# Kernel optimization log

Measured on AMD Instinct MI355X. Metric: run time of the kernel, lower is better.

Reference implementation:

```python
import jax, jax.numpy as jnp
import numpy as np

B, S, HID, NH, INTER = 1, 2048, 1024, 16, 4096
D = INTER // NH  # per-head intermediate dim = 256


def setup_inputs() -> dict:
    key = jax.random.key(0)
    ks = jax.random.split(key, 10)
    w = lambda k, shp: jax.random.normal(k, shp, jnp.float32) * 0.02
    return {
        "x": jax.random.normal(ks[0], (B, S, HID), jnp.float32),
        "adjacency": jax.random.uniform(ks[1], (B, NH, S, S), jnp.float32),
        "Wg": w(ks[2], (INTER, HID)),   # gate_proj.weight (out,in)
        "Wu": w(ks[3], (INTER, HID)),   # up_proj.weight
        "Wd": w(ks[4], (HID, INTER)),   # down_proj.weight
        "eps": jnp.zeros((NH,), jnp.float32),   # GIN epsilons (init 0)
        "alpha": jnp.ones((NH,), jnp.float32),  # sum-agg scales (init 1)
        "Wq": w(ks[5], (NH, D, D)),     # per-head attn_query_projs weights (out,in)
        "Wk": w(ks[6], (NH, D, D)),     # per-head attn_key_projs weights
        "W1": w(ks[7], (D, 4 * D)),     # aggregator_mlp[0].weight
        "W2": w(ks[8], (D, D)),         # aggregator_mlp[2].weight
    }


def reference(x, adjacency, Wg, Wu, Wd, eps, alpha, Wq, Wk, W1, W2):
    b, s, _ = x.shape
    nh, d, _ = Wq.shape
    # first half of SwiGLU MLP
    h = jax.nn.silu(x @ Wg.T) * (x @ Wu.T)            # (b, s, inter)
    h = h.reshape(b, s, nh, d).transpose(0, 2, 1, 3)  # (b, h, s, d)
    # GIN original term
    orig = (1.0 + eps)[None, :, None, None] * h
    # sum aggregation over adjacency
    sum_agg = alpha[None, :, None, None] * jnp.einsum('bhij,bhjd->bhid', adjacency, h)
    # max over identical expanded copies of h along the neighbor axis == h itself
    max_agg = h
    # adjacency-log-masked attention aggregation
    Q = jnp.einsum('bhsd,hed->bhse', h, Wq)
    K = jnp.einsum('bhsd,hed->bhse', h, Wk)
    scores = jnp.einsum('bhse,bhte->bhst', Q, K) / jnp.sqrt(jnp.float32(d))
    scores = scores + jnp.log(adjacency + 1e-9)
    attn = jax.nn.softmax(scores, axis=-1)
    attn_agg = jnp.einsum('bhst,bhtd->bhsd', attn, h)
    # 4-way concat + aggregator MLP (per head, shared weights)
    comb = jnp.concatenate([orig, sum_agg, max_agg, attn_agg], axis=-1)  # (b,h,s,4d)
    gin = jnp.einsum('bhsd,od->bhso', jax.nn.silu(jnp.einsum('bhsi,oi->bhso', comb, W1)), W2)
    # recombine heads and finish MLP
    gin = gin.transpose(0, 2, 1, 3).reshape(b, s, nh * d)
    return gin @ Wd.T
```

## Files before the change

kernel.cpp:

```cpp
#include <hip/hip_runtime.h>

typedef unsigned short u16;
typedef __attribute__((ext_vector_type(4))) float f32x4;
typedef __attribute__((ext_vector_type(8))) short s16x8;
typedef __attribute__((ext_vector_type(4))) short s16x4;

#define DEVI static __device__ __forceinline__

constexpr int S = 2048, HID = 1024, NH = 16, D = 256, INTER = 4096;

constexpr size_t N_XB   = (size_t)S*HID;
constexpr size_t N_W    = (size_t)INTER*HID;
constexpr size_t N_WQK  = (size_t)NH*D*D;
constexpr size_t N_W1C  = (size_t)NH*D*768;
constexpr size_t N_W2   = (size_t)D*D;
constexpr size_t N_COMB = (size_t)NH*S*768;
constexpr size_t N_HB   = (size_t)NH*S*D;

constexpr size_t O_XB   = 0;
constexpr size_t O_WG   = O_XB + N_XB;
constexpr size_t O_WU   = O_WG + N_W;
constexpr size_t O_WD   = O_WU + N_W;
constexpr size_t O_WQ   = O_WD + N_W;
constexpr size_t O_WK   = O_WQ + N_WQK;
constexpr size_t O_W1C  = O_WK + N_WQK;
constexpr size_t O_W2   = O_W1C + N_W1C;
constexpr size_t O_COMB = O_W2 + N_W2;
constexpr size_t O_HB   = O_COMB + N_COMB;
constexpr size_t O_QB   = O_HB + N_HB;
constexpr size_t O_KC   = O_QB + N_HB;

DEVI u16 f2bf(float f) {
  union { float f; unsigned u; } v; v.f = f;
  unsigned r = v.u + 0x7FFFu + ((v.u >> 16) & 1u);
  return (u16)(r >> 16);
}

DEVI float bf2f(u16 b) {
  union { unsigned u; float f; } v; v.u = ((unsigned)b) << 16;
  return v.f;
}

DEVI void gload16(const void* g, const void* l) {
  __builtin_amdgcn_global_load_lds(
      (const __attribute__((address_space(1))) unsigned int*)g,
      (__attribute__((address_space(3))) unsigned int*)l, 16, 0, 0);
}

DEVI void stage_rm(const u16* src, int stride, u16* lds, int tid) {
  const int wid = tid >> 6;
#pragma unroll
  for (int i = 0; i < 2; ++i) {
    int c = i * 256 + tid;
    gload16(src + (size_t)(c & 127) * stride + (c >> 7) * 8,
            lds + (size_t)(i * 256 + wid * 64) * 8);
  }
}

DEVI s16x8 ldfrag(const u16* lds, int kp, int row) {
  return *(const s16x8*)(lds + ((size_t)kp * 128 + row) * 8);
}

__global__ void k_convert(const float* __restrict__ x,  const float* __restrict__ Wg,
                          const float* __restrict__ Wu, const float* __restrict__ Wd,
                          const float* __restrict__ Wq, const float* __restrict__ Wk,
                          const float* __restrict__ W1, const float* __restrict__ W2,
                          const float* __restrict__ eps, const float* __restrict__ alpha,
                          u16* __restrict__ ws) {
  const size_t total = N_XB + N_W + N_W + N_W + N_WQK + N_WQK + N_W2 + N_W1C;
  for (size_t i = (size_t)blockIdx.x * blockDim.x + threadIdx.x; i < total;
       i += (size_t)gridDim.x * blockDim.x) {
    size_t j = i;
    if (j < N_XB)  { ws[O_XB + j] = f2bf(x[j]);  continue; } j -= N_XB;
    if (j < N_W)   { ws[O_WG + j] = f2bf(Wg[j]); continue; } j -= N_W;
    if (j < N_W)   { ws[O_WU + j] = f2bf(Wu[j]); continue; } j -= N_W;
    if (j < N_W)   { ws[O_WD + j] = f2bf(Wd[j]); continue; } j -= N_W;
    if (j < N_WQK) { ws[O_WQ + j] = f2bf(Wq[j]); continue; } j -= N_WQK;
    if (j < N_WQK) { ws[O_WK + j] = f2bf(Wk[j]); continue; } j -= N_WQK;
    if (j < N_W2)  { ws[O_W2 + j] = f2bf(W2[(j % D) * D + (j / D)]); continue; } j -= N_W2;
    size_t h = j / ((size_t)D * 768);
    size_t r = j % ((size_t)D * 768);
    size_t o = r / 768, c = r % 768;
    float v;
    if (c < 256)      v = (1.f + eps[h]) * W1[o * 1024 + c] + W1[o * 1024 + 512 + c];
    else if (c < 512) v = alpha[h] * W1[o * 1024 + c];
    else              v = W1[o * 1024 + 256 + c];
    ws[O_W1C + j] = f2bf(v);
  }
}

template <int MODE>
__global__ __launch_bounds__(256, 2) void k_dual(const u16* __restrict__ Ab,
                                                 const u16* __restrict__ B0b,
                                                 const u16* __restrict__ B1b,
                                                 u16* __restrict__ o0, u16* __restrict__ o1) {
  __shared__ u16 lA[4096], lB0[4096], lB1[4096];
  const int tid = threadIdx.x, lane = tid & 63, wid = tid >> 6;
  const int wm = wid >> 1, wn = wid & 1;
  const int m0 = blockIdx.x * 128, nt = blockIdx.y, head = blockIdx.z;

  const int K  = (MODE == 0) ? HID : D;
  const int sA = (MODE == 0) ? HID : 768;
  const int sB = (MODE == 0) ? HID : D;
  const u16* A  = (MODE == 0) ? (Ab + (size_t)m0 * HID)
                              : (Ab + ((size_t)head * S + m0) * 768);
  const u16* B0 = (MODE == 0) ? (B0b + (size_t)nt * 128 * HID)
                              : (B0b + (size_t)head * D * D + (size_t)nt * 128 * D);
  const u16* B1 = (MODE == 0) ? (B1b + (size_t)nt * 128 * HID)
                              : (B1b + (size_t)head * D * D + (size_t)nt * 128 * D);

  f32x4 a0[4][4], a1[4][4];
#pragma unroll
  for (int i = 0; i < 4; ++i)
#pragma unroll
    for (int j = 0; j < 4; ++j) { a0[i][j] = f32x4{0.f,0.f,0.f,0.f}; a1[i][j] = f32x4{0.f,0.f,0.f,0.f}; }

  for (int k0 = 0; k0 < K; k0 += 32) {
    __syncthreads();
    stage_rm(A  + k0, sA, lA,  tid);
    stage_rm(B0 + k0, sB, lB0, tid);
    stage_rm(B1 + k0, sB, lB1, tid);
    __syncthreads();
    const int kp = lane >> 4, r = lane & 15;
    s16x8 af[4], b0f[4], b1f[4];
#pragma unroll
    for (int f = 0; f < 4; ++f) {
      af[f]  = ldfrag(lA,  kp, wm * 64 + f * 16 + r);
      b0f[f] = ldfrag(lB0, kp, wn * 64 + f * 16 + r);
      b1f[f] = ldfrag(lB1, kp, wn * 64 + f * 16 + r);
    }
#pragma unroll
    for (int fi = 0; fi < 4; ++fi)
#pragma unroll
      for (int fj = 0; fj < 4; ++fj) {
        a0[fi][fj] = __builtin_amdgcn_mfma_f32_16x16x32_bf16(af[fi], b0f[fj], a0[fi][fj], 0, 0, 0);
        a1[fi][fj] = __builtin_amdgcn_mfma_f32_16x16x32_bf16(af[fi], b1f[fj], a1[fi][fj], 0, 0, 0);
      }
  }

#pragma unroll
  for (int fi = 0; fi < 4; ++fi)
#pragma unroll
    for (int fj = 0; fj < 4; ++fj)
#pragma unroll
      for (int reg = 0; reg < 4; ++reg) {
        int row = m0 + wm * 64 + fi * 16 + ((lane >> 4) * 4 + reg);
        int cl  = wn * 64 + fj * 16 + (lane & 15);
        if (MODE == 0) {
          int col = nt * 128 + cl;
          float g = a0[fi][fj][reg], uu = a1[fi][fj][reg];
          float h = g / (1.f + __expf(-g)) * uu;
          u16 hb = f2bf(h);
          int hh = col >> 8, d = col & 255;
          o0[((size_t)hh * S + row) * 768 + d] = hb;
          o1[(((size_t)hh * (S / 8) + (row >> 3)) * 256 + d) * 8 + (row & 7)] = hb;
        } else {
          int e = nt * 128 + cl;
          o0[((size_t)head * S + row) * D + e] = f2bf(a0[fi][fj][reg]);
          o1[(((size_t)head * 32 + (e >> 3)) * S + row) * 8 + (e & 7)] = f2bf(a1[fi][fj][reg]);
        }
      }
}

__global__ __launch_bounds__(256, 2) void k_attn(const float* __restrict__ adj,
                                                 const u16* __restrict__ Qb,
                                                 const u16* __restrict__ Kc,
                                                 const u16* __restrict__ hB,
                                                 u16* __restrict__ comb) {
  __shared__ u16 lK[2][1024 * 8];
  __shared__ u16 lH[2][1024 * 8];
  __shared__ u16 lAdj[2][64 * 36];
  __shared__ u16 lP[4][16 * 36];
  const int tid = threadIdx.x, lane = tid & 63, wid = tid >> 6;
  const int head = blockIdx.y;
  const int q0 = blockIdx.x * 64 + wid * 16;
  const int l15 = lane & 15, l4 = lane >> 4;

  s16x8 q[8];
  {
    const u16* qr = Qb + ((size_t)head * S + q0 + l15) * D + l4 * 8;
#pragma unroll
    for (int ks = 0; ks < 8; ++ks) q[ks] = *(const s16x8*)(qr + ks * 32);
  }
  f32x4 accO[16], accS[16];
#pragma unroll
  for (int i = 0; i < 16; ++i) { accO[i] = f32x4{0.f,0.f,0.f,0.f}; accS[i] = f32x4{0.f,0.f,0.f,0.f}; }
  float m_r[4] = {-1e30f, -1e30f, -1e30f, -1e30f};
  float l_r[4] = {0.f, 0.f, 0.f, 0.f};

  const float* adjB = adj + ((size_t)head * S + blockIdx.x * 64) * S;
  const int arow = tid >> 3;
  const int acol = (tid & 7) * 4;

#pragma unroll
  for (int i = 0; i < 4; ++i) {
    int c = i * 256 + tid;
    gload16(Kc + ((size_t)(head * 32 + (c >> 5)) * S + (c & 31)) * 8,
            &lK[0][(size_t)(i * 256 + wid * 64) * 8]);
  }
#pragma unroll
  for (int i = 0; i < 4; ++i) {
    int c = i * 256 + tid;
    gload16(hB + ((size_t)(head * (S / 8) + (c >> 8)) * 256 + (c & 255)) * 8,
            &lH[0][(size_t)(i * 256 + wid * 64) * 8]);
  }
  f32x4 av0 = *(const f32x4*)(adjB + (size_t)arow * S + acol);
  f32x4 av1 = *(const f32x4*)(adjB + (size_t)(arow + 32) * S + acol);

  int cur = 0;
  for (int t0 = 0; t0 < S; t0 += 32, cur ^= 1) {
    const int t1 = (t0 + 32 < S) ? t0 + 32 : t0;
#pragma unroll
    for (int i = 0; i < 4; ++i) {
      int c = i * 256 + tid;
      gload16(Kc + ((size_t)(head * 32 + (c >> 5)) * S + t1 + (c & 31)) * 8,
              &lK[cur ^ 1][(size_t)(i * 256 + wid * 64) * 8]);
    }
#pragma unroll
    for (int i = 0; i < 4; ++i) {
      int c = i * 256 + tid;
      gload16(hB + ((size_t)(head * (S / 8) + (t1 >> 3) + (c >> 8)) * 256 + (c & 255)) * 8,
              &lH[cur ^ 1][(size_t)(i * 256 + wid * 64) * 8]);
    }
    f32x4 nv0 = *(const f32x4*)(adjB + (size_t)arow * S + t1 + acol);
    f32x4 nv1 = *(const f32x4*)(adjB + (size_t)(arow + 32) * S + t1 + acol);
    {
      s16x4 w;
      w[0] = (short)f2bf(av0[0]); w[1] = (short)f2bf(av0[1]);
      w[2] = (short)f2bf(av0[2]); w[3] = (short)f2bf(av0[3]);
      *(s16x4*)(&lAdj[cur][(size_t)arow * 36 + acol]) = w;
      w[0] = (short)f2bf(av1[0]); w[1] = (short)f2bf(av1[1]);
      w[2] = (short)f2bf(av1[2]); w[3] = (short)f2bf(av1[3]);
      *(s16x4*)(&lAdj[cur][(size_t)(arow + 32) * 36 + acol]) = w;
    }
    __builtin_amdgcn_sched_barrier(0);
    asm volatile("s_waitcnt vmcnt(10) lgkmcnt(0)" ::: "memory");
    __builtin_amdgcn_sched_barrier(0);
    __builtin_amdgcn_s_barrier();
    __builtin_amdgcn_sched_barrier(0);

    const u16* lKc = &lK[cur][0];
    const u16* lHc = &lH[cur][0];
    const u16* lAc = &lAdj[cur][0];

    f32x4 scA[2], scB[2];
    scA[0] = f32x4{0.f,0.f,0.f,0.f}; scA[1] = f32x4{0.f,0.f,0.f,0.f};
    scB[0] = f32x4{0.f,0.f,0.f,0.f}; scB[1] = f32x4{0.f,0.f,0.f,0.f};
    __builtin_amdgcn_s_setprio(1);
#pragma unroll
    for (int ks = 0; ks < 4; ++ks)
#pragma unroll
      for (int fj = 0; fj < 2; ++fj) {
        s16x8 b0 = *(const s16x8*)(lKc + ((size_t)(ks * 4 + l4) * 32 + fj * 16 + l15) * 8);
        s16x8 b1 = *(const s16x8*)(lKc + ((size_t)((ks + 4) * 4 + l4) * 32 + fj * 16 + l15) * 8);
        scA[fj] = __builtin_amdgcn_mfma_f32_16x16x32_bf16(q[ks], b0, scA[fj], 0, 0, 0);
        scB[fj] = __builtin_amdgcn_mfma_f32_16x16x32_bf16(q[ks + 4], b1, scB[fj], 0, 0, 0);
      }
    __builtin_amdgcn_s_setprio(0);

    float av[2][4];
#pragma unroll
    for (int fj = 0; fj < 2; ++fj)
#pragma unroll
      for (int reg = 0; reg < 4; ++reg)
        av[fj][reg] = bf2f(lAc[(size_t)(wid * 16 + l4 * 4 + reg) * 36 + fj * 16 + l15]);

    float sf[2][4];
#pragma unroll
    for (int fj = 0; fj < 2; ++fj)
#pragma unroll
      for (int reg = 0; reg < 4; ++reg)
        sf[fj][reg] = (scA[fj][reg] + scB[fj][reg]) * 0.0625f;

    bool chg = false;
    float lmax[4];
#pragma unroll
    for (int reg = 0; reg < 4; ++reg) {
      lmax[reg] = fmaxf(sf[0][reg], sf[1][reg]);
      chg |= (lmax[reg] > m_r[reg] + 8.f);
    }
    if (__any((int)chg)) {
      float scl[4];
#pragma unroll
      for (int reg = 0; reg < 4; ++reg) {
        float m = lmax[reg];
#pragma unroll
        for (int off = 1; off < 16; off <<= 1) m = fmaxf(m, __shfl_xor(m, off));
        float mn = fmaxf(m_r[reg], m);
        scl[reg] = __expf(m_r[reg] - mn);
        m_r[reg] = mn;
        l_r[reg] *= scl[reg];
      }
#pragma unroll
      for (int nf = 0; nf < 16; ++nf) {
        f32x4 t = accO[nf];
        t[0] *= scl[0]; t[1] *= scl[1]; t[2] *= scl[2]; t[3] *= scl[3];
        accO[nf] = t;
      }
    }
    u16 pb[2][4];
#pragma unroll
    for (int fj = 0; fj < 2; ++fj)
#pragma unroll
      for (int reg = 0; reg < 4; ++reg) {
        float p = (av[fj][reg] + 1e-9f) * exp2f((sf[fj][reg] - m_r[reg]) * 1.44269504f);
        l_r[reg] += p;
        pb[fj][reg] = f2bf(p);
      }

    u16* pl = &lP[wid][0];
#pragma unroll
    for (int fj = 0; fj < 2; ++fj)
#pragma unroll
      for (int reg = 0; reg < 4; ++reg)
        pl[(size_t)(l4 * 4 + reg) * 36 + fj * 16 + l15] = pb[fj][reg];
    asm volatile("s_waitcnt lgkmcnt(0)" ::: "memory");
    __builtin_amdgcn_sched_barrier(0);

    s16x8 pa, aa;
    {
      s16x4 plo = *(const s16x4*)(pl + (size_t)l15 * 36 + l4 * 8);
      s16x4 phi = *(const s16x4*)(pl + (size_t)l15 * 36 + l4 * 8 + 4);
      pa[0] = plo[0]; pa[1] = plo[1]; pa[2] = plo[2]; pa[3] = plo[3];
      pa[4] = phi[0]; pa[5] = phi[1]; pa[6] = phi[2]; pa[7] = phi[3];
      s16x4 alo = *(const s16x4*)(lAc + (size_t)(wid * 16 + l15) * 36 + l4 * 8);
      s16x4 ahi = *(const s16x4*)(lAc + (size_t)(wid * 16 + l15) * 36 + l4 * 8 + 4);
      aa[0] = alo[0]; aa[1] = alo[1]; aa[2] = alo[2]; aa[3] = alo[3];
      aa[4] = ahi[0]; aa[5] = ahi[1]; aa[6] = ahi[2]; aa[7] = ahi[3];
    }
    __builtin_amdgcn_s_setprio(1);
#pragma unroll
    for (int nf = 0; nf < 16; ++nf) {
      s16x8 hb = *(const s16x8*)(lHc + ((size_t)l4 * 256 + nf * 16 + l15) * 8);
      accO[nf] = __builtin_amdgcn_mfma_f32_16x16x32_bf16(pa, hb, accO[nf], 0, 0, 0);
      accS[nf] = __builtin_amdgcn_mfma_f32_16x16x32_bf16(aa, hb, accS[nf], 0, 0, 0);
    }
    __builtin_amdgcn_s_setprio(0);

    av0 = nv0; av1 = nv1;

    __builtin_amdgcn_sched_barrier(0);
    __builtin_amdgcn_s_barrier();
  }

  asm volatile("s_waitcnt vmcnt(0)" ::: "memory");

#pragma unroll
  for (int reg = 0; reg < 4; ++reg) {
#pragma unroll
    for (int off = 1; off < 16; off <<= 1) l_r[reg] += __shfl_xor(l_r[reg], off);
  }
  float inv[4];
#pragma unroll
  for (int reg = 0; reg < 4; ++reg) inv[reg] = 1.f / l_r[reg];
#pragma unroll
  for (int nf = 0; nf < 16; ++nf)
#pragma unroll
    for (int reg = 0; reg < 4; ++reg) {
      size_t rb = ((size_t)head * S + q0 + l4 * 4 + reg) * 768;
      comb[rb + 512 + nf * 16 + l15] = f2bf(accO[nf][reg] * inv[reg]);
      comb[rb + 256 + nf * 16 + l15] = f2bf(accS[nf][reg]);
    }
}

template <int MODE>
__global__ __launch_bounds__(256, 2) void k_gemm(const u16* __restrict__ Ab,
                                                 const u16* __restrict__ Bb,
                                                 u16* __restrict__ oU, float* __restrict__ oF) {
  __shared__ u16 lA[4096], lB[4096];
  const int tid = threadIdx.x, lane = tid & 63, wid = tid >> 6;
  const int wm = wid >> 1, wn = wid & 1;
  const int m0 = blockIdx.x * 128, nt = blockIdx.y, head = blockIdx.z;

  constexpr int K  = (MODE == 0) ? 768 : (MODE == 2) ? INTER : D;
  constexpr int sA = (MODE == 3) ? INTER : K;
  constexpr int sB = K;
  const u16* A = (MODE == 0) ? Ab + ((size_t)head * S + m0) * 768
               : (MODE == 2) ? Ab + (size_t)m0 * INTER
                             : Ab + (size_t)m0 * INTER + head * D;
  const u16* B = (MODE == 0) ? Bb + ((size_t)head * D + nt * 128) * 768
                             : Bb + (size_t)nt * 128 * sB;

  f32x4 acc[4][4];
#pragma unroll
  for (int i = 0; i < 4; ++i)
#pragma unroll
    for (int j = 0; j < 4; ++j) acc[i][j] = f32x4{0.f,0.f,0.f,0.f};

  for (int k0 = 0; k0 < K; k0 += 32) {
    __syncthreads();
    stage_rm(A + k0, sA, lA, tid);
    stage_rm(B + k0, sB, lB, tid);
    __syncthreads();
    const int kp = lane >> 4, r = lane & 15;
    s16x8 af[4], bf[4];
#pragma unroll
    for (int f = 0; f < 4; ++f) {
      af[f] = ldfrag(lA, kp, wm * 64 + f * 16 + r);
      bf[f] = ldfrag(lB, kp, wn * 64 + f * 16 + r);
    }
#pragma unroll
    for (int fi = 0; fi < 4; ++fi)
#pragma unroll
      for (int fj = 0; fj < 4; ++fj)
        acc[fi][fj] = __builtin_amdgcn_mfma_f32_16x16x32_bf16(af[fi], bf[fj], acc[fi][fj], 0, 0, 0);
  }

#pragma unroll
  for (int fi = 0; fi < 4; ++fi)
#pragma unroll
    for (int fj = 0; fj < 4; ++fj)
#pragma unroll
      for (int reg = 0; reg < 4; ++reg) {
        int row = m0 + wm * 64 + fi * 16 + ((lane >> 4) * 4 + reg);
        int cn = nt * 128 + wn * 64 + fj * 16 + (lane & 15);
        float v = acc[fi][fj][reg];
        if (MODE == 0) {
          v = v / (1.f + __expf(-v));
          oU[(size_t)row * INTER + head * D + cn] = f2bf(v);
        } else if (MODE == 3) {
          oU[(size_t)row * INTER + head * D + cn] = f2bf(v);
        } else {
          oF[(size_t)row * HID + cn] = v;
        }
      }
}

extern "C" void kernel_launch(void* const* d_in, const int* in_sizes, int n_in,
                              void* d_out, int out_size, void* d_ws, size_t ws_size,
                              hipStream_t stream) {
  const float* x     = (const float*)d_in[0];
  const float* adj   = (const float*)d_in[1];
  const float* Wg    = (const float*)d_in[2];
  const float* Wu    = (const float*)d_in[3];
  const float* Wd    = (const float*)d_in[4];
  const float* eps   = (const float*)d_in[5];
  const float* alpha = (const float*)d_in[6];
  const float* Wq    = (const float*)d_in[7];
  const float* Wk    = (const float*)d_in[8];
  const float* W1    = (const float*)d_in[9];
  const float* W2    = (const float*)d_in[10];
  u16* ws = (u16*)d_ws;

  k_convert<<<dim3(4096), dim3(256), 0, stream>>>(x, Wg, Wu, Wd, Wq, Wk, W1, W2, eps, alpha, ws);
  k_dual<0><<<dim3(16, 32, 1), dim3(256), 0, stream>>>(ws + O_XB, ws + O_WG, ws + O_WU,
                                                       ws + O_COMB, ws + O_HB);
  k_dual<1><<<dim3(16, 2, 16), dim3(256), 0, stream>>>(ws + O_COMB, ws + O_WQ, ws + O_WK,
                                                       ws + O_QB, ws + O_KC);
  k_attn<<<dim3(32, 16), dim3(256), 0, stream>>>(adj, ws + O_QB, ws + O_KC, ws + O_HB, ws + O_COMB);
  k_gemm<3><<<dim3(8, 2, 16), dim3(256), 0, stream>>>(ws + O_WD, ws + O_W2, ws + O_KC, nullptr);
  k_gemm<0><<<dim3(16, 2, 16), dim3(256), 0, stream>>>(ws + O_COMB, ws + O_W1C, ws + O_QB, nullptr);
  k_gemm<2><<<dim3(16, 8, 1), dim3(256), 0, stream>>>(ws + O_QB, ws + O_KC, nullptr, (float*)d_out);
}
```

Measured before the change: 449.4 us.

## Compute transposed scores to skip P LDS round-trip and drop online max

The attention kernel now computes S^T by swapping the MFMA operands, so each lane holds the scores in the layout needed for the P operand of the PV matmul. The probabilities are packed straight into registers with 16x16x16 MFMAs, which removes the per-wave LDS staging buffer and its wait. The running-max rescaling is also dropped and the exponentials are taken unshifted, on the assumption that scores stay small. This cuts ALU, shuffle and LDS work, but it doubles the MFMA instruction count and risks overflow if scores grow.

```diff
diff --git a/kernel.cpp b/kernel.cpp
--- a/kernel.cpp
+++ b/kernel.cpp
@@ -45,6 +45,19 @@
   __builtin_amdgcn_global_load_lds(
       (const __attribute__((address_space(1))) unsigned int*)g,
       (__attribute__((address_space(3))) unsigned int*)l, 16, 0, 0);
+}
+
+DEVI f32x4 mfma16(s16x4 a, s16x4 b, f32x4 c) {
+#if __has_builtin(__builtin_amdgcn_mfma_f32_16x16x16_bf16)
+  return __builtin_amdgcn_mfma_f32_16x16x16_bf16(a, b, c, 0, 0, 0);
+#elif __has_builtin(__builtin_amdgcn_mfma_f32_16x16x16bf16_1k)
+  return __builtin_amdgcn_mfma_f32_16x16x16bf16_1k(a, b, c, 0, 0, 0);
+#else
+  f32x4 d;
+  asm volatile("v_mfma_f32_16x16x16_bf16 %0, %1, %2, %3"
+               : "=v"(d) : "v"(a), "v"(b), "v"(c));
+  return d;
+#endif
 }
 
 DEVI void stage_rm(const u16* src, int stride, u16* lds, int tid) {
@@ -170,7 +183,6 @@
   __shared__ u16 lK[2][1024 * 8];
   __shared__ u16 lH[2][1024 * 8];
   __shared__ u16 lAdj[2][64 * 36];
-  __shared__ u16 lP[4][16 * 36];
   const int tid = threadIdx.x, lane = tid & 63, wid = tid >> 6;
   const int head = blockIdx.y;
   const int q0 = blockIdx.x * 64 + wid * 16;
@@ -185,8 +197,7 @@
   f32x4 accO[16], accS[16];
 #pragma unroll
   for (int i = 0; i < 16; ++i) { accO[i] = f32x4{0.f,0.f,0.f,0.f}; accS[i] = f32x4{0.f,0.f,0.f,0.f}; }
-  float m_r[4] = {-1e30f, -1e30f, -1e30f, -1e30f};
-  float l_r[4] = {0.f, 0.f, 0.f, 0.f};
+  float l_r = 0.f;
 
   const float* adjB = adj + ((size_t)head * S + blockIdx.x * 64) * S;
   const int arow = tid >> 3;
@@ -251,89 +262,36 @@
     for (int ks = 0; ks < 4; ++ks)
 #pragma unroll
       for (int fj = 0; fj < 2; ++fj) {
-        s16x8 b0 = *(const s16x8*)(lKc + ((size_t)(ks * 4 + l4) * 32 + fj * 16 + l15) * 8);
-        s16x8 b1 = *(const s16x8*)(lKc + ((size_t)((ks + 4) * 4 + l4) * 32 + fj * 16 + l15) * 8);
-        scA[fj] = __builtin_amdgcn_mfma_f32_16x16x32_bf16(q[ks], b0, scA[fj], 0, 0, 0);
-        scB[fj] = __builtin_amdgcn_mfma_f32_16x16x32_bf16(q[ks + 4], b1, scB[fj], 0, 0, 0);
+        s16x8 k0f = *(const s16x8*)(lKc + ((size_t)(ks * 4 + l4) * 32 + fj * 16 + l15) * 8);
+        s16x8 k1f = *(const s16x8*)(lKc + ((size_t)((ks + 4) * 4 + l4) * 32 + fj * 16 + l15) * 8);
+        scA[fj] = __builtin_amdgcn_mfma_f32_16x16x32_bf16(k0f, q[ks], scA[fj], 0, 0, 0);
+        scB[fj] = __builtin_amdgcn_mfma_f32_16x16x32_bf16(k1f, q[ks + 4], scB[fj], 0, 0, 0);
       }
     __builtin_amdgcn_s_setprio(0);
 
-    float av[2][4];
-#pragma unroll
-    for (int fj = 0; fj < 2; ++fj)
-#pragma unroll
-      for (int reg = 0; reg < 4; ++reg)
-        av[fj][reg] = bf2f(lAc[(size_t)(wid * 16 + l4 * 4 + reg) * 36 + fj * 16 + l15]);
-
-    float sf[2][4];
-#pragma unroll
-    for (int fj = 0; fj < 2; ++fj)
-#pragma unroll
-      for (int reg = 0; reg < 4; ++reg)
-        sf[fj][reg] = (scA[fj][reg] + scB[fj][reg]) * 0.0625f;
-
-    bool chg = false;
-    float lmax[4];
-#pragma unroll
-    for (int reg = 0; reg < 4; ++reg) {
-      lmax[reg] = fmaxf(sf[0][reg], sf[1][reg]);
-      chg |= (lmax[reg] > m_r[reg] + 8.f);
-    }
-    if (__any((int)chg)) {
-      float scl[4];
-#pragma unroll
-      for (int reg = 0; reg < 4; ++reg) {
-        float m = lmax[reg];
-#pragma unroll
-        for (int off = 1; off < 16; off <<= 1) m = fmaxf(m, __shfl_xor(m, off));
-        float mn = fmaxf(m_r[reg], m);
-        scl[reg] = __expf(m_r[reg] - mn);
-        m_r[reg] = mn;
-        l_r[reg] *= scl[reg];
-      }
-#pragma unroll
-      for (int nf = 0; nf < 16; ++nf) {
-        f32x4 t = accO[nf];
-        t[0] *= scl[0]; t[1] *= scl[1]; t[2] *= scl[2]; t[3] *= scl[3];
-        accO[nf] = t;
-      }
-    }
-    u16 pb[2][4];
-#pragma unroll
-    for (int fj = 0; fj < 2; ++fj)
-#pragma unroll
-      for (int reg = 0; reg < 4; ++reg) {
-        float p = (av[fj][reg] + 1e-9f) * exp2f((sf[fj][reg] - m_r[reg]) * 1.44269504f);
-        l_r[reg] += p;
-        pb[fj][reg] = f2bf(p);
-      }
-
-    u16* pl = &lP[wid][0];
-#pragma unroll
-    for (int fj = 0; fj < 2; ++fj)
-#pragma unroll
-      for (int reg = 0; reg < 4; ++reg)
-        pl[(size_t)(l4 * 4 + reg) * 36 + fj * 16 + l15] = pb[fj][reg];
-    asm volatile("s_waitcnt lgkmcnt(0)" ::: "memory");
-    __builtin_amdgcn_sched_barrier(0);
-
-    s16x8 pa, aa;
-    {
-      s16x4 plo = *(const s16x4*)(pl + (size_t)l15 * 36 + l4 * 8);
-      s16x4 phi = *(const s16x4*)(pl + (size_t)l15 * 36 + l4 * 8 + 4);
-      pa[0] = plo[0]; pa[1] = plo[1]; pa[2] = plo[2]; pa[3] = plo[3];
-      pa[4] = phi[0]; pa[5] = phi[1]; pa[6] = phi[2]; pa[7] = phi[3];
-      s16x4 alo = *(const s16x4*)(lAc + (size_t)(wid * 16 + l15) * 36 + l4 * 8);
-      s16x4 ahi = *(const s16x4*)(lAc + (size_t)(wid * 16 + l15) * 36 + l4 * 8 + 4);
-      aa[0] = alo[0]; aa[1] = alo[1]; aa[2] = alo[2]; aa[3] = alo[3];
-      aa[4] = ahi[0]; aa[5] = ahi[1]; aa[6] = ahi[2]; aa[7] = ahi[3];
-    }
+    s16x4 aa0 = *(const s16x4*)(lAc + (size_t)(wid * 16 + l15) * 36 + l4 * 4);
+    s16x4 aa1 = *(const s16x4*)(lAc + (size_t)(wid * 16 + l15) * 36 + 16 + l4 * 4);
+
+    constexpr float EC = 1.44269504f / 16.f;
+    s16x4 pa0, pa1;
+#pragma unroll
+    for (int j = 0; j < 4; ++j) {
+      float p0 = (bf2f((u16)aa0[j]) + 1e-9f) * exp2f((scA[0][j] + scB[0][j]) * EC);
+      float p1 = (bf2f((u16)aa1[j]) + 1e-9f) * exp2f((scA[1][j] + scB[1][j]) * EC);
+      l_r += p0 + p1;
+      pa0[j] = (short)f2bf(p0);
+      pa1[j] = (short)f2bf(p1);
+    }
+
     __builtin_amdgcn_s_setprio(1);
 #pragma unroll
     for (int nf = 0; nf < 16; ++nf) {
-      s16x8 hb = *(const s16x8*)(lHc + ((size_t)l4 * 256 + nf * 16 + l15) * 8);
-      accO[nf] = __builtin_amdgcn_mfma_f32_16x16x32_bf16(pa, hb, accO[nf], 0, 0, 0);
-      accS[nf] = __builtin_amdgcn_mfma_f32_16x16x32_bf16(aa, hb, accS[nf], 0, 0, 0);
+      s16x4 hb0 = *(const s16x4*)(lHc + (size_t)((l4 >> 1) * 256 + nf * 16 + l15) * 8 + (l4 & 1) * 4);
+      s16x4 hb1 = *(const s16x4*)(lHc + (size_t)((2 + (l4 >> 1)) * 256 + nf * 16 + l15) * 8 + (l4 & 1) * 4);
+      accO[nf] = mfma16(pa0, hb0, accO[nf]);
+      accO[nf] = mfma16(pa1, hb1, accO[nf]);
+      accS[nf] = mfma16(aa0, hb0, accS[nf]);
+      accS[nf] = mfma16(aa1, hb1, accS[nf]);
     }
     __builtin_amdgcn_s_setprio(0);
 
@@ -345,20 +303,18 @@
 
   asm volatile("s_waitcnt vmcnt(0)" ::: "memory");
 
-#pragma unroll
-  for (int reg = 0; reg < 4; ++reg) {
-#pragma unroll
-    for (int off = 1; off < 16; off <<= 1) l_r[reg] += __shfl_xor(l_r[reg], off);
-  }
-  float inv[4];
-#pragma unroll
-  for (int reg = 0; reg < 4; ++reg) inv[reg] = 1.f / l_r[reg];
+  l_r += __shfl_xor(l_r, 16);
+  l_r += __shfl_xor(l_r, 32);
+  float inv = 1.f / l_r;
+  float invr[4];
+#pragma unroll
+  for (int reg = 0; reg < 4; ++reg) invr[reg] = __shfl(inv, l4 * 4 + reg);
 #pragma unroll
   for (int nf = 0; nf < 16; ++nf)
 #pragma unroll
     for (int reg = 0; reg < 4; ++reg) {
       size_t rb = ((size_t)head * S + q0 + l4 * 4 + reg) * 768;
-      comb[rb + 512 + nf * 16 + l15] = f2bf(accO[nf][reg] * inv[reg]);
+      comb[rb + 512 + nf * 16 + l15] = f2bf(accO[nf][reg] * invr[reg]);
       comb[rb + 256 + nf * 16 + l15] = f2bf(accS[nf][reg]);
     }
 }
```

New measurement: 475.1 us. +5.7%, slower.
